# Kernel optimization log

Hardware: AMD Instinct MI355X
Metric: run time of the kernel (lower is better)

The kernel has to match this reference:

```python
import jax, jax.numpy as jnp
import numpy as np

B, S, D = 4, 2048, 768
H = 12
HD = D // H  # 64
SCALE = HD ** -0.5

def setup_inputs() -> dict:
    key = jax.random.key(0)
    k1, k2, k3 = jax.random.split(key, 3)
    x = jax.random.normal(k1, (B, S, D), dtype=jnp.float32)
    w_qkv = jax.random.normal(k2, (D, 3 * D), dtype=jnp.float32) * (D ** -0.5)
    w_out = jax.random.normal(k3, (D, D), dtype=jnp.float32) * (D ** -0.5)
    b_out = jnp.zeros((D,), dtype=jnp.float32)
    return {"x": x, "w_qkv": w_qkv, "w_out": w_out, "b_out": b_out}

def reference(x, w_qkv, w_out, b_out):
    B_, S_, D_ = x.shape
    # qkv projection (no bias), then 'b s (qkv h d) -> qkv b h s d'
    qkv = (x @ w_qkv).reshape(B_, S_, 3, H, HD).transpose(2, 0, 3, 1, 4)
    q, k, v = qkv[0], qkv[1], qkv[2]  # each [B, H, S, HD]
    att = jnp.einsum('bhxd,bhyd->bhxy', q, k) * SCALE
    att = jax.nn.softmax(att, axis=-1)  # dropout_rate=0 -> identity
    out = jnp.einsum('bhxy,bhyd->bhxd', att, v)
    out = out.transpose(0, 2, 1, 3).reshape(B_, S_, D_)  # 'b h s d -> b s (h d)'
    return out @ w_out + b_out
```

## Files before the change

### kernel.cpp

```cpp
#include <hip/hip_runtime.h>

#define BB 4
#define SS 2048
#define DD 768
#define HH 12
#define HDIM 64

using bf16_t = __bf16;
typedef __bf16 bf16x8 __attribute__((ext_vector_type(8)));
typedef __bf16 bf16x4 __attribute__((ext_vector_type(4)));
typedef float f32x4 __attribute__((ext_vector_type(4)));
typedef unsigned int u32;

static __device__ __forceinline__ void cp16(void* lds, const void* g) {
  __builtin_amdgcn_global_load_lds(
      (const __attribute__((address_space(1))) u32*)g,
      (__attribute__((address_space(3))) u32*)lds, 16, 0, 0);
}

__global__ void cvt_x(const float* __restrict__ in, bf16_t* __restrict__ out) {
  const size_t i = ((size_t)blockIdx.x * 256 + threadIdx.x) * 8;
  f32x4 f0 = *(const f32x4*)(in + i);
  f32x4 f1 = *(const f32x4*)(in + i + 4);
  bf16x8 v;
#pragma unroll
  for (int j = 0; j < 4; j++) { v[j] = (bf16_t)f0[j]; v[4 + j] = (bf16_t)f1[j]; }
  *(bf16x8*)(out + i) = v;
}

__global__ void wt_transpose(const float* __restrict__ in, bf16_t* __restrict__ out,
                             int K, int N) {
  __shared__ bf16_t tile[64][65];
  const int n0 = blockIdx.x * 64, k0 = blockIdx.y * 64;
  const int t = threadIdx.x;
  const int r = t >> 2;
  const int c0 = (t & 3) * 16;
  const float* src = in + (size_t)(k0 + r) * N + n0 + c0;
#pragma unroll
  for (int q = 0; q < 4; q++) {
    f32x4 f = *(const f32x4*)(src + q * 4);
#pragma unroll
    for (int j = 0; j < 4; j++) tile[r][c0 + q * 4 + j] = (bf16_t)f[j];
  }
  __syncthreads();
  bf16x8 o0, o1;
#pragma unroll
  for (int j = 0; j < 8; j++) { o0[j] = tile[c0 + j][r]; o1[j] = tile[c0 + 8 + j][r]; }
  *(bf16x8*)(out + (size_t)(n0 + r) * K + k0 + c0) = o0;
  *(bf16x8*)(out + (size_t)(n0 + r) * K + k0 + c0 + 8) = o1;
}

template <int MODE>
__global__ __launch_bounds__(256, 4)
void gemm_bt(const bf16_t* __restrict__ A, const bf16_t* __restrict__ Bt,
             int M, int N, int K,
             bf16_t* __restrict__ q_out, bf16_t* __restrict__ k_out,
             bf16_t* __restrict__ vt_out,
             float* __restrict__ Cout, const float* __restrict__ bias) {
  __shared__ bf16_t As[128][64];
  __shared__ bf16_t Bs[128][64];
  const int t = threadIdx.x;
  const int lane = t & 63, wave = t >> 6;
  const int l15 = lane & 15, quad = lane >> 4;
  const int wm = (wave >> 1) * 64, wn = (wave & 1) * 64;
  const int m0 = blockIdx.y * 128, n0 = blockIdx.x * 128;
  const int srow = lane >> 3;
  const int schunk = ((lane & 7) ^ srow) * 8;
  const int rsw = l15 & 7;

  f32x4 acc[4][4];
#pragma unroll
  for (int i = 0; i < 4; i++)
#pragma unroll
    for (int j = 0; j < 4; j++) acc[i][j] = (f32x4){0.f, 0.f, 0.f, 0.f};

  for (int k0 = 0; k0 < K; k0 += 64) {
    __syncthreads();
#pragma unroll
    for (int p = 0; p < 4; p++) {
      const int row = wave * 32 + p * 8 + srow;
      const bf16_t* asrc;
      if (MODE == 0) {
        asrc = A + (size_t)(m0 + row) * K + k0 + schunk;
      } else {
        const int mm = m0 + row, b = mm >> 11, s = mm & 2047, h = k0 >> 6;
        asrc = A + (((size_t)(b * HH + h)) * SS + s) * HDIM + schunk;
      }
      cp16(&As[wave * 32 + p * 8][0], asrc);
      cp16(&Bs[wave * 32 + p * 8][0],
           Bt + (size_t)(n0 + row) * K + k0 + schunk);
    }
    __syncthreads();
#pragma unroll
    for (int kk = 0; kk < 2; kk++) {
      bf16x8 af[4], bfr[4];
#pragma unroll
      for (int i = 0; i < 4; i++)
        af[i] = *(const bf16x8*)&As[wm + i * 16 + l15][((kk * 4 + quad) ^ rsw) * 8];
#pragma unroll
      for (int j = 0; j < 4; j++)
        bfr[j] = *(const bf16x8*)&Bs[wn + j * 16 + l15][((kk * 4 + quad) ^ rsw) * 8];
#pragma unroll
      for (int i = 0; i < 4; i++)
#pragma unroll
        for (int j = 0; j < 4; j++)
          acc[i][j] = __builtin_amdgcn_mfma_f32_16x16x32_bf16(af[i], bfr[j], acc[i][j], 0, 0, 0);
    }
  }

  const float QSCALE = 0.125f * 1.44269504088896340736f;
#pragma unroll
  for (int i = 0; i < 4; i++) {
    const int mbase = m0 + wm + i * 16 + quad * 4;
#pragma unroll
    for (int j = 0; j < 4; j++) {
      const int n = n0 + wn + j * 16 + l15;
#pragma unroll
      for (int r = 0; r < 4; r++) {
        const float v = acc[i][j][r];
        const int mm = mbase + r;
        if (MODE == 0) {
          const int sel = n / DD;
          const int rem = n - sel * DD;
          const int h = rem >> 6, d = rem & 63;
          const int b = mm >> 11, s = mm & 2047;
          if (sel == 2) {
            const int sp = (s & ~63) | (((s & 15) << 2) | ((s >> 4) & 3));
            vt_out[((size_t)(b * HH + h) * HDIM + d) * SS + sp] = (bf16_t)v;
          } else {
            const size_t idx = (((size_t)(b * HH + h)) * SS + s) * HDIM + d;
            if (sel == 0) q_out[idx] = (bf16_t)(v * QSCALE);
            else k_out[idx] = (bf16_t)v;
          }
        } else {
          Cout[(size_t)mm * N + n] = v + bias[n];
        }
      }
    }
  }
}

__global__ __launch_bounds__(256, 3)
void attn_kernel(bf16_t* __restrict__ Qio, const bf16_t* __restrict__ Kg,
                 const bf16_t* __restrict__ Vt) {
  __shared__ bf16_t Ks[2][64][64];
  __shared__ bf16_t Vts[2][64][64];
  __shared__ bf16_t Ps[128][64];
  const int t = threadIdx.x;
  const int lane = t & 63, wave = t >> 6;
  const int l15 = lane & 15, quad = lane >> 4;
  const int bh = blockIdx.y;
  const int q0 = blockIdx.x * 128;
  const size_t base = (size_t)bh * SS * HDIM;
  const size_t baset = (size_t)bh * HDIM * SS;
  const int wq = wave * 32;
  const int srow = lane >> 3;
  const int schunk = ((lane & 7) ^ srow) * 8;
  const int rsw = l15 & 7;

  bf16x8 qf[2][2];
#pragma unroll
  for (int rt = 0; rt < 2; rt++)
#pragma unroll
    for (int kh = 0; kh < 2; kh++)
      qf[rt][kh] = *(const bf16x8*)(Qio + base + (size_t)(q0 + wq + rt * 16 + l15) * HDIM +
                                    kh * 32 + quad * 8);

  float l_loc[2][4];
  f32x4 o_acc[2][4];
#pragma unroll
  for (int rt = 0; rt < 2; rt++) {
#pragma unroll
    for (int r = 0; r < 4; r++) l_loc[rt][r] = 0.f;
#pragma unroll
    for (int dt = 0; dt < 4; dt++) o_acc[rt][dt] = (f32x4){0.f, 0.f, 0.f, 0.f};
  }

  auto stage = [&](int k0, int buf) {
#pragma unroll
    for (int p = 0; p < 2; p++) {
      const int row = wave * 16 + p * 8 + srow;
      cp16(&Ks[buf][wave * 16 + p * 8][0],
           Kg + base + (size_t)(k0 + row) * HDIM + schunk);
      cp16(&Vts[buf][wave * 16 + p * 8][0],
           Vt + baset + (size_t)row * SS + k0 + schunk);
    }
  };

  stage(0, 0);

  for (int it = 0; it < SS / 64; it++) {
    const int buf = it & 1;
    __syncthreads();

    f32x4 s_acc[2][4];
#pragma unroll
    for (int rt = 0; rt < 2; rt++)
#pragma unroll
      for (int ct = 0; ct < 4; ct++) s_acc[rt][ct] = (f32x4){0.f, 0.f, 0.f, 0.f};
#pragma unroll
    for (int kh = 0; kh < 2; kh++) {
#pragma unroll
      for (int ct = 0; ct < 4; ct++) {
        bf16x8 kf = *(const bf16x8*)&Ks[buf][ct * 16 + l15][((kh * 4 + quad) ^ rsw) * 8];
#pragma unroll
        for (int rt = 0; rt < 2; rt++)
          s_acc[rt][ct] = __builtin_amdgcn_mfma_f32_16x16x32_bf16(qf[rt][kh], kf, s_acc[rt][ct], 0, 0, 0);
      }
    }

#pragma unroll
    for (int rt = 0; rt < 2; rt++) {
#pragma unroll
      for (int r = 0; r < 4; r++) {
        const float p0 = __builtin_amdgcn_exp2f(s_acc[rt][0][r]);
        const float p1 = __builtin_amdgcn_exp2f(s_acc[rt][1][r]);
        const float p2 = __builtin_amdgcn_exp2f(s_acc[rt][2][r]);
        const float p3 = __builtin_amdgcn_exp2f(s_acc[rt][3][r]);
        l_loc[rt][r] += (p0 + p1) + (p2 + p3);
        bf16x4 pk = {(bf16_t)p0, (bf16_t)p1, (bf16_t)p2, (bf16_t)p3};
        const int row = wq + rt * 16 + quad * 4 + r;
        *(bf16x4*)&Ps[row][((l15 >> 1) ^ (row & 7)) * 8 + (l15 & 1) * 4] = pk;
      }
    }

    __syncthreads();

    if (it + 1 < SS / 64) stage((it + 1) * 64, buf ^ 1);

#pragma unroll
    for (int kh = 0; kh < 2; kh++) {
      bf16x8 pf[2];
#pragma unroll
      for (int rt = 0; rt < 2; rt++)
        pf[rt] = *(const bf16x8*)&Ps[wq + rt * 16 + l15][((kh * 4 + quad) ^ rsw) * 8];
#pragma unroll
      for (int dt = 0; dt < 4; dt++) {
        bf16x8 vf = *(const bf16x8*)&Vts[buf][dt * 16 + l15][((kh * 4 + quad) ^ rsw) * 8];
#pragma unroll
        for (int rt = 0; rt < 2; rt++)
          o_acc[rt][dt] = __builtin_amdgcn_mfma_f32_16x16x32_bf16(pf[rt], vf, o_acc[rt][dt], 0, 0, 0);
      }
    }
  }

#pragma unroll
  for (int rt = 0; rt < 2; rt++) {
#pragma unroll
    for (int r = 0; r < 4; r++) {
      float l = l_loc[rt][r];
#pragma unroll
      for (int off = 1; off < 16; off <<= 1) l += __shfl_xor(l, off);
      const float inv = 1.0f / l;
      const int s = q0 + wq + rt * 16 + quad * 4 + r;
#pragma unroll
      for (int dt = 0; dt < 4; dt++) {
        const int d = dt * 16 + l15;
        Qio[base + (size_t)s * HDIM + d] = (bf16_t)(o_acc[rt][dt][r] * inv);
      }
    }
  }
}

extern "C" void kernel_launch(void* const* d_in, const int* in_sizes, int n_in,
                              void* d_out, int out_size, void* d_ws, size_t ws_size,
                              hipStream_t stream) {
  const float* x = (const float*)d_in[0];
  const float* w_qkv = (const float*)d_in[1];
  const float* w_out = (const float*)d_in[2];
  const float* b_out = (const float*)d_in[3];
  float* out = (float*)d_out;

  char* ws = (char*)d_ws;
  bf16_t* wqkv_t = (bf16_t*)ws; ws += (size_t)3 * DD * DD * 2;
  bf16_t* wout_t = (bf16_t*)ws; ws += (size_t)DD * DD * 2;
  bf16_t* q_ws = (bf16_t*)ws;   ws += (size_t)BB * HH * SS * HDIM * 2;
  bf16_t* k_ws = (bf16_t*)ws;
  bf16_t* vt_sc = (bf16_t*)d_out;
  bf16_t* xb = (bf16_t*)d_out + (size_t)BB * SS * DD;

  cvt_x<<<(BB * SS * DD) / (256 * 8), 256, 0, stream>>>(x, xb);
  wt_transpose<<<dim3(3 * DD / 64, DD / 64), 256, 0, stream>>>(w_qkv, wqkv_t, DD, 3 * DD);
  wt_transpose<<<dim3(DD / 64, DD / 64), 256, 0, stream>>>(w_out, wout_t, DD, DD);
  gemm_bt<0><<<dim3(3 * DD / 128, BB * SS / 128), 256, 0, stream>>>(
      xb, wqkv_t, BB * SS, 3 * DD, DD, q_ws, k_ws, vt_sc, nullptr, nullptr);
  attn_kernel<<<dim3(SS / 128, BB * HH), 256, 0, stream>>>(q_ws, k_ws, vt_sc);
  gemm_bt<1><<<dim3(DD / 128, BB * SS / 128), 256, 0, stream>>>(
      q_ws, wout_t, BB * SS, DD, DD, nullptr, nullptr, nullptr, out, b_out);
}
```

Measured before the change: 224.9 us.

## Remap blocks per XCD for L2 locality and compute softmax row sums via MFMA

Both GEMMs and the attention kernel now use a flat 1D grid. Block IDs are remapped so that consecutive blocks dispatched round-robin to the same XCD share M rows (GEMM) or the same batch-head (attention), which is meant to improve per-XCD L2 reuse of K/V and A tiles. The softmax denominator is no longer accumulated with scalar adds and a cross-lane shuffle reduction. It is instead computed by an extra MFMA of P against a ones vector, moving that VALU work onto the matrix units. The sum now uses the bf16-rounded P values, which matches the numerator, but it adds two MFMAs per k-half.

New measurement: 229.2 us. Within noise of the previous version (+1.9%).

```diff
diff --git a/kernel.cpp b/kernel.cpp
--- a/kernel.cpp
+++ b/kernel.cpp
@@ -50,7 +50,7 @@
   *(bf16x8*)(out + (size_t)(n0 + r) * K + k0 + c0 + 8) = o1;
 }
 
-template <int MODE>
+template <int MODE, int NT>
 __global__ __launch_bounds__(256, 4)
 void gemm_bt(const bf16_t* __restrict__ A, const bf16_t* __restrict__ Bt,
              int M, int N, int K,
@@ -63,7 +63,9 @@
   const int lane = t & 63, wave = t >> 6;
   const int l15 = lane & 15, quad = lane >> 4;
   const int wm = (wave >> 1) * 64, wn = (wave & 1) * 64;
-  const int m0 = blockIdx.y * 128, n0 = blockIdx.x * 128;
+  const int bid = blockIdx.x;
+  const int xcd = bid & 7, q = bid >> 3;
+  const int m0 = (xcd * 8 + q / NT) * 128, n0 = (q % NT) * 128;
   const int srow = lane >> 3;
   const int schunk = ((lane & 7) ^ srow) * 8;
   const int rsw = l15 & 7;
@@ -149,8 +151,10 @@
   const int t = threadIdx.x;
   const int lane = t & 63, wave = t >> 6;
   const int l15 = lane & 15, quad = lane >> 4;
-  const int bh = blockIdx.y;
-  const int q0 = blockIdx.x * 128;
+  const int bid = blockIdx.x;
+  const int xcd = bid & 7, qq = bid >> 3;
+  const int bh = xcd * 6 + qq / 16;
+  const int q0 = (qq % 16) * 128;
   const size_t base = (size_t)bh * SS * HDIM;
   const size_t baset = (size_t)bh * HDIM * SS;
   const int wq = wave * 32;
@@ -166,12 +170,14 @@
       qf[rt][kh] = *(const bf16x8*)(Qio + base + (size_t)(q0 + wq + rt * 16 + l15) * HDIM +
                                     kh * 32 + quad * 8);
 
-  float l_loc[2][4];
-  f32x4 o_acc[2][4];
+  bf16x8 ones;
+#pragma unroll
+  for (int j = 0; j < 8; j++) ones[j] = (bf16_t)1.0f;
+
+  f32x4 o_acc[2][4], l_acc[2];
 #pragma unroll
   for (int rt = 0; rt < 2; rt++) {
-#pragma unroll
-    for (int r = 0; r < 4; r++) l_loc[rt][r] = 0.f;
+    l_acc[rt] = (f32x4){0.f, 0.f, 0.f, 0.f};
 #pragma unroll
     for (int dt = 0; dt < 4; dt++) o_acc[rt][dt] = (f32x4){0.f, 0.f, 0.f, 0.f};
   }
@@ -217,7 +223,6 @@
         const float p1 = __builtin_amdgcn_exp2f(s_acc[rt][1][r]);
         const float p2 = __builtin_amdgcn_exp2f(s_acc[rt][2][r]);
         const float p3 = __builtin_amdgcn_exp2f(s_acc[rt][3][r]);
-        l_loc[rt][r] += (p0 + p1) + (p2 + p3);
         bf16x4 pk = {(bf16_t)p0, (bf16_t)p1, (bf16_t)p2, (bf16_t)p3};
         const int row = wq + rt * 16 + quad * 4 + r;
         *(bf16x4*)&Ps[row][((l15 >> 1) ^ (row & 7)) * 8 + (l15 & 1) * 4] = pk;
@@ -241,6 +246,9 @@
         for (int rt = 0; rt < 2; rt++)
           o_acc[rt][dt] = __builtin_amdgcn_mfma_f32_16x16x32_bf16(pf[rt], vf, o_acc[rt][dt], 0, 0, 0);
       }
+#pragma unroll
+      for (int rt = 0; rt < 2; rt++)
+        l_acc[rt] = __builtin_amdgcn_mfma_f32_16x16x32_bf16(pf[rt], ones, l_acc[rt], 0, 0, 0);
     }
   }
 
@@ -248,10 +256,7 @@
   for (int rt = 0; rt < 2; rt++) {
 #pragma unroll
     for (int r = 0; r < 4; r++) {
-      float l = l_loc[rt][r];
-#pragma unroll
-      for (int off = 1; off < 16; off <<= 1) l += __shfl_xor(l, off);
-      const float inv = 1.0f / l;
+      const float inv = 1.0f / l_acc[rt][r];
       const int s = q0 + wq + rt * 16 + quad * 4 + r;
 #pragma unroll
       for (int dt = 0; dt < 4; dt++) {
@@ -282,9 +287,9 @@
   cvt_x<<<(BB * SS * DD) / (256 * 8), 256, 0, stream>>>(x, xb);
   wt_transpose<<<dim3(3 * DD / 64, DD / 64), 256, 0, stream>>>(w_qkv, wqkv_t, DD, 3 * DD);
   wt_transpose<<<dim3(DD / 64, DD / 64), 256, 0, stream>>>(w_out, wout_t, DD, DD);
-  gemm_bt<0><<<dim3(3 * DD / 128, BB * SS / 128), 256, 0, stream>>>(
+  gemm_bt<0, 18><<<8 * 8 * 18, 256, 0, stream>>>(
       xb, wqkv_t, BB * SS, 3 * DD, DD, q_ws, k_ws, vt_sc, nullptr, nullptr);
-  attn_kernel<<<dim3(SS / 128, BB * HH), 256, 0, stream>>>(q_ws, k_ws, vt_sc);
-  gemm_bt<1><<<dim3(DD / 128, BB * SS / 128), 256, 0, stream>>>(
+  attn_kernel<<<8 * 6 * 16, 256, 0, stream>>>(q_ws, k_ws, vt_sc);
+  gemm_bt<1, 6><<<8 * 8 * 6, 256, 0, stream>>>(
       q_ws, wout_t, BB * SS, DD, DD, nullptr, nullptr, nullptr, out, b_out);
 }
```
